# Kernel optimization log

Hardware: AMD Instinct MI355X
Metric: run time of the kernel (lower is better)

## Reference

```python
import jax, jax.numpy as jnp
import numpy as np
import math

CODE_NUM = 8192
GRAPH = 256
HID = 256
ATT = 128
TOUT = 256  # must equal HID (scattered into h_new)


def setup_inputs() -> dict:
    key = jax.random.key(0)
    ks = jax.random.split(key, 16)
    s = 0.02
    return {
        "m_embeddings": jax.random.normal(ks[0], (CODE_NUM, GRAPH), jnp.float32),
        "ddi_embeddings": jax.random.normal(ks[1], (CODE_NUM, GRAPH), jnp.float32),
        "unrelated_embeddings": jax.random.normal(ks[2], (CODE_NUM, GRAPH), jnp.float32),
        "hidden_state": jax.random.normal(ks[3], (CODE_NUM, HID), jnp.float32),
        # GRUCell params (torch layout: W_ih [3H, in], W_hh [3H, H])
        "W_ih": jax.random.normal(ks[4], (3 * HID, GRAPH), jnp.float32) * s,
        "W_hh": jax.random.normal(ks[5], (3 * HID, HID), jnp.float32) * s,
        "b_ih": jax.random.normal(ks[6], (3 * HID,), jnp.float32) * s,
        "b_hh": jax.random.normal(ks[7], (3 * HID,), jnp.float32) * s,
        # single-head attention params ([in, out] layout)
        "Wq": jax.random.normal(ks[8], (GRAPH, ATT), jnp.float32) * s,
        "bq": jax.random.normal(ks[9], (ATT,), jnp.float32) * s,
        "Wk": jax.random.normal(ks[10], (GRAPH, ATT), jnp.float32) * s,
        "bk": jax.random.normal(ks[11], (ATT,), jnp.float32) * s,
        "Wv": jax.random.normal(ks[12], (GRAPH, TOUT), jnp.float32) * s,
        "bv": jax.random.normal(ks[13], (TOUT,), jnp.float32) * s,
        # categorical group id per code: 0 -> m1 (GRU), 1 -> m2 (ddi), 2 -> m3 (unrelated)
        "divided": jax.random.randint(ks[14], (CODE_NUM,), 0, 3, jnp.int32),
    }


def reference(m_embeddings, ddi_embeddings, unrelated_embeddings, hidden_state,
              W_ih, W_hh, b_ih, b_hh, Wq, bq, Wk, bk, Wv, bv, divided):
    m1 = divided == 0
    m2 = divided == 1
    m3 = divided == 2
    m23 = m2 | m3

    # ---- GRUCell on all rows (row-independent); scatter only m1 rows ----
    gx = m_embeddings @ W_ih.T + b_ih          # [N, 3H]
    gh = hidden_state @ W_hh.T + b_hh          # [N, 3H]
    xr, xz, xn = jnp.split(gx, 3, axis=-1)
    hr, hz, hn = jnp.split(gh, 3, axis=-1)
    r = jax.nn.sigmoid(xr + hr)
    z = jax.nn.sigmoid(xz + hz)
    n = jnp.tanh(xn + r * hn)
    h_gru = (1.0 - z) * n + z * hidden_state   # [N, H]

    # ---- single-head attention over m2 u m3 subset (mask-based) ----
    q_in = jnp.where(m2[:, None], ddi_embeddings, unrelated_embeddings)  # [N, G]
    Q = q_in @ Wq + bq                          # [N, A]
    K = q_in @ Wk + bk                          # [N, A]
    V = m_embeddings @ Wv + bv                  # [N, TOUT]
    g = (Q @ K.T) / math.sqrt(ATT)              # [N, N]
    g = jnp.where(m23[None, :], g, -jnp.inf)    # keys restricted to m2 u m3
    score = jax.nn.softmax(g, axis=-1)
    h_m23 = jnp.tanh(score @ V)                 # [N, H]

    # ---- scatter into h_new ----
    h_new = jnp.where(m1[:, None], h_gru, 0.0)
    h_new = jnp.where(m23[:, None], h_m23, h_new)

    # ---- max-pooled outputs over each subset, then combined ----
    out1 = jnp.max(jnp.where(m1[:, None], h_gru, -jnp.inf), axis=0)    # [H]
    out23 = jnp.max(jnp.where(m23[:, None], h_m23, -jnp.inf), axis=0)  # [H]
    output = jnp.maximum(out1, out23)
    return output, h_new
```

## Files before the change

kernel.cpp:

```cpp
#include <hip/hip_runtime.h>

typedef __bf16 bf16_t;
typedef __bf16 bf16x8 __attribute__((ext_vector_type(8)));
typedef float f32x4 __attribute__((ext_vector_type(4)));

#define MFMA16(A, B, C) __builtin_amdgcn_mfma_f32_16x16x32_bf16(A, B, C, 0, 0, 0)

static constexpr int N_CODE = 8192;

static constexpr size_t OFF_B1   = 0;
static constexpr size_t OFF_B2   = OFF_B1 + 393216;
static constexpr size_t OFF_B3   = OFF_B2 + 393216;
static constexpr size_t OFF_BV   = OFF_B3 + 131072;
static constexpr size_t OFF_BIAS = OFF_BV + 131072;
static constexpr size_t OFF_U1   = OFF_BIAS + 8192;
static constexpr size_t OFF_U23  = OFF_U1 + 1024;
static constexpr size_t OFF_CNT  = OFF_U23 + 1024;
static constexpr size_t OFF_IDXS = OFF_CNT + 256;
static constexpr size_t OFF_IDXM = OFF_IDXS + 32768;
static constexpr size_t OFF_GXC  = OFF_IDXM + 32768;
static constexpr size_t OFF_GHC  = OFF_GXC + 12582912;
static constexpr size_t OFF_G3C  = OFF_GHC + 12582912;
static constexpr size_t OFF_VT   = OFF_G3C + 4194304;
static constexpr size_t OFF_KP   = OFF_VT + 4194304;
static constexpr size_t OFF_VP   = OFF_KP + 2097152;
static constexpr size_t OFF_PML  = OFF_VP + 4194304;
static constexpr size_t OFF_PO   = OFF_PML + 524288;

__device__ __forceinline__ unsigned umap_f(float f) {
    unsigned u = __float_as_uint(f);
    return (u & 0x80000000u) ? ~u : (u | 0x80000000u);
}
__device__ __forceinline__ float unmap_f(unsigned u) {
    unsigned b = (u & 0x80000000u) ? (u & 0x7fffffffu) : ~u;
    return __uint_as_float(b);
}

__global__ __launch_bounds__(1024)
void tl_prep_scan(const float* __restrict__ W_ih, const float* __restrict__ W_hh,
                  const float* __restrict__ Wq, const float* __restrict__ Wk,
                  const float* __restrict__ Wv,
                  const float* __restrict__ b_ih, const float* __restrict__ b_hh,
                  const float* __restrict__ bq, const float* __restrict__ bk,
                  const float* __restrict__ bv,
                  const int* __restrict__ divided,
                  bf16_t* __restrict__ B1p, bf16_t* __restrict__ B2p,
                  bf16_t* __restrict__ B3p, bf16_t* __restrict__ BVp,
                  float* __restrict__ biases,
                  unsigned* __restrict__ u1, unsigned* __restrict__ u23,
                  int* __restrict__ idxS, int* __restrict__ idxM1, int* __restrict__ counts)
{
    int t = threadIdx.x;
    if (blockIdx.x == 0) {
        __shared__ int w1[16], w23[16];
        int lane = t & 63, wv = t >> 6;
        int d[8]; int c1 = 0, c23 = 0;
#pragma unroll
        for (int i = 0; i < 8; ++i) {
            d[i] = divided[t*8 + i];
            c1  += (d[i] == 0);
            c23 += (d[i] != 0);
        }
        int s1v = c1, s23v = c23;
#pragma unroll
        for (int off = 1; off < 64; off <<= 1) {
            int a1  = __shfl_up(s1v,  off, 64);
            int a23 = __shfl_up(s23v, off, 64);
            if (lane >= off) { s1v += a1; s23v += a23; }
        }
        if (lane == 63) { w1[wv] = s1v; w23[wv] = s23v; }
        __syncthreads();
        if (wv == 0 && lane < 16) {
            int v1 = w1[lane], v23 = w23[lane];
#pragma unroll
            for (int off = 1; off < 16; off <<= 1) {
                int a1  = __shfl_up(v1,  off, 16);
                int a23 = __shfl_up(v23, off, 16);
                if (lane >= off) { v1 += a1; v23 += a23; }
            }
            w1[lane] = v1; w23[lane] = v23;
        }
        __syncthreads();
        int base1  = (wv > 0) ? w1[wv-1]  : 0;
        int base23 = (wv > 0) ? w23[wv-1] : 0;
        int o1  = base1  + s1v  - c1;
        int o23 = base23 + s23v - c23;
#pragma unroll
        for (int i = 0; i < 8; ++i) {
            if (d[i] == 0) idxM1[o1++] = t*8 + i;
            else           idxS[o23++] = t*8 + i;
        }
        if (t == 1023) { counts[0] = w23[15]; counts[1] = w1[15]; }
        return;
    }
    int idx = (blockIdx.x - 1) * 1024 + t;
    const int T1 = 196608, T2 = 196608, T3 = 65536, T4 = 65536;
    for (int i = idx; i < T1 + T2 + T3 + T4; i += 128 * 1024) {
        int which, l;
        if (i < T1)                { which = 0; l = i; }
        else if (i < T1 + T2)      { which = 1; l = i - T1; }
        else if (i < T1 + T2 + T3) { which = 2; l = i - T1 - T2; }
        else                       { which = 3; l = i - T1 - T2 - T3; }
        int j = l & 7, lane = (l >> 3) & 63, kk = (l >> 9) & 7, n16 = l >> 12;
        int k = kk*32 + (lane >> 4)*8 + j;
        int n = n16*16 + (lane & 15);
        if (which == 0)      B1p[l] = (bf16_t)W_ih[n*256 + k];
        else if (which == 1) B2p[l] = (bf16_t)W_hh[n*256 + k];
        else if (which == 2) B3p[l] = (bf16_t)((n < 128) ? Wq[k*128 + n] : Wk[k*128 + (n - 128)]);
        else                 BVp[l] = (bf16_t)Wv[k*256 + n];
    }
    if (idx < 768)       biases[idx] = b_ih[idx];
    else if (idx < 1536) biases[idx] = b_hh[idx - 768];
    else if (idx < 1792) { int q = idx - 1536; biases[idx] = (q < 128) ? bq[q] : bk[q - 128]; }
    else if (idx < 2048) biases[idx] = bv[idx - 1792];
    if (idx < 256) { u1[idx] = 0x007FFFFFu; u23[idx] = 0x007FFFFFu; }
}

__device__ __forceinline__ bf16x8 load_cvt8(const float* p) {
    f32x4 a = *(const f32x4*)p;
    f32x4 b = *(const f32x4*)(p + 4);
    bf16x8 r;
#pragma unroll
    for (int j = 0; j < 4; ++j) { r[j] = (bf16_t)a[j]; r[j+4] = (bf16_t)b[j]; }
    return r;
}

__global__ __launch_bounds__(256, 2)
void tl_gemm_quad(const float* __restrict__ m_emb, const float* __restrict__ hidden,
                  const float* __restrict__ ddi, const float* __restrict__ unrel,
                  const int* __restrict__ divided,
                  const bf16_t* __restrict__ B1p, const bf16_t* __restrict__ B2p,
                  const bf16_t* __restrict__ B3p, const bf16_t* __restrict__ BVp,
                  const float* __restrict__ biases,
                  bf16_t* __restrict__ gxc, bf16_t* __restrict__ ghc,
                  bf16_t* __restrict__ G3c, bf16_t* __restrict__ Vt,
                  const int* __restrict__ idxM1, const int* __restrict__ idxS,
                  const int* __restrict__ counts)
{
    int y = blockIdx.y;
    const float* A0; const float* A1 = nullptr; int mode = 0;
    const bf16_t* Bp; const float* bias; bf16_t* C; int NOUT; int y0;
    const int* gidx; int cnt;
    if (y < 3)       { A0 = m_emb;  gidx = idxM1; cnt = counts[1]; Bp = B1p; bias = biases;        C = gxc; NOUT = 768; y0 = y; }
    else if (y < 6)  { A0 = hidden; gidx = idxM1; cnt = counts[1]; Bp = B2p; bias = biases + 768;  C = ghc; NOUT = 768; y0 = y - 3; }
    else if (y == 6) { A0 = ddi; A1 = unrel; mode = 2;
                       gidx = idxS;  cnt = counts[0]; Bp = B3p; bias = biases + 1536; C = G3c; NOUT = 256; y0 = 0; }
    else             { A0 = m_emb;  gidx = idxS;  cnt = counts[0]; Bp = BVp; bias = biases + 1792; C = Vt;  NOUT = 256; y0 = 0; }

    int m0 = blockIdx.x * 64;
    if (m0 >= cnt) return;
    int lane = threadIdx.x & 63;
    int w    = threadIdx.x >> 6;
    int rlo = lane & 15, khi = lane >> 4;
    int nbase = y0 * 256 + w * 64;

    const float* arow[4];
#pragma unroll
    for (int m = 0; m < 4; ++m) {
        int row = m0 + m*16 + rlo;
        int src = gidx[(row < cnt) ? row : 0];
        const float* base = A0;
        if (mode == 2) base = (divided[src] == 1) ? A0 : A1;
        arow[m] = base + (size_t)src * 256;
    }
    f32x4 acc[4][4] = {};
    const bf16_t* bptr = Bp + (size_t)(nbase >> 4) * 4096 + lane * 8;
#pragma unroll
    for (int kk = 0; kk < 8; ++kk) {
        bf16x8 bfrag[4];
#pragma unroll
        for (int nf = 0; nf < 4; ++nf)
            bfrag[nf] = *(const bf16x8*)(bptr + nf * 4096 + kk * 512);
#pragma unroll
        for (int m = 0; m < 4; ++m) {
            bf16x8 afrag = load_cvt8(arow[m] + kk*32 + khi*8);
#pragma unroll
            for (int nf = 0; nf < 4; ++nf)
                acc[m][nf] = MFMA16(afrag, bfrag[nf], acc[m][nf]);
        }
    }
#pragma unroll
    for (int nf = 0; nf < 4; ++nf) {
        int col = nbase + nf*16 + rlo;
        float b = bias[col];
#pragma unroll
        for (int m = 0; m < 4; ++m)
#pragma unroll
            for (int r = 0; r < 4; ++r) {
                int row = m0 + m*16 + khi*4 + r;
                C[(size_t)row * NOUT + col] = (bf16_t)(acc[m][nf][r] + b);
            }
    }
}

__global__ __launch_bounds__(256)
void tl_gru_pack(const bf16_t* __restrict__ gx, const bf16_t* __restrict__ gh,
                 const float* __restrict__ hidden,
                 const int* __restrict__ idxM1, const int* __restrict__ counts,
                 float* __restrict__ h_new, unsigned* __restrict__ u1,
                 const bf16_t* __restrict__ G3c, const bf16_t* __restrict__ Vt,
                 bf16_t* __restrict__ Kp, bf16_t* __restrict__ Vp)
{
    if (blockIdx.x < 1024) {
        int nM1 = counts[1];
        int i0 = blockIdx.x * 8;
        if (i0 >= nM1) return;
        int j = threadIdx.x;
        int iend = (i0 + 8 < nM1) ? i0 + 8 : nM1;
        float cmax = -1e30f;
        for (int i = i0; i < iend; ++i) {
            int row = idxM1[i];
            float xr = (float)gx[(size_t)i*768 + j];
            float xz = (float)gx[(size_t)i*768 + 256 + j];
            float xn = (float)gx[(size_t)i*768 + 512 + j];
            float hr = (float)gh[(size_t)i*768 + j];
            float hz = (float)gh[(size_t)i*768 + 256 + j];
            float hn = (float)gh[(size_t)i*768 + 512 + j];
            float h  = hidden[(size_t)row*256 + j];
            float r = 1.f/(1.f + __expf(-(xr + hr)));
            float z = 1.f/(1.f + __expf(-(xz + hz)));
            float n = tanhf(xn + r*hn);
            float hg = (1.f - z)*n + z*h;
            h_new[(size_t)row*256 + j] = hg;
            cmax = fmaxf(cmax, hg);
        }
        atomicMax(&u1[j], umap_f(cmax));
        return;
    }
    int nS = counts[0];
    int nT = (nS + 63) >> 6;
    int r = (blockIdx.x - 1024) * 4 + (threadIdx.x >> 6);
    if (r >= nT * 64) return;
    int t = threadIdx.x & 63;
    bool valid = r < nS;
    if (t < 16) {
        bf16x8 v = {};
        if (valid) v = *(const bf16x8*)(G3c + (size_t)r*256 + 128 + t*8);
        int kt = r >> 6, keyin = r & 63;
        int ks = t >> 2, lhi = t & 3, nf = keyin >> 4;
        int lane = (lhi << 4) | (keyin & 15);
        *(bf16x8*)(Kp + ((((size_t)kt*4 + ks)*4 + nf)*64 + lane)*8) = v;
    } else if (t < 48) {
        int j8 = t - 16;
        int d0 = j8 * 8;
        bf16x8 v = {};
        if (valid) v = *(const bf16x8*)(Vt + (size_t)r*256 + d0);
        int kt = r >> 6, ks2 = (r >> 5) & 1, jj = r & 7, lhi = (r >> 3) & 3;
#pragma unroll
        for (int q = 0; q < 8; ++q) {
            int d = d0 + q;
            int nf = d >> 4;
            int lane = (lhi << 4) | (d & 15);
            Vp[((((size_t)kt*2 + ks2)*16 + nf)*64 + lane)*8 + jj] = v[q];
        }
    }
}

__global__ __launch_bounds__(256, 2)
void tl_attn(const bf16_t* __restrict__ G3c, const bf16_t* __restrict__ Kp,
             const bf16_t* __restrict__ Vp, const int* __restrict__ counts,
             int ksplit, float* __restrict__ pml, bf16_t* __restrict__ pO)
{
    int nS = counts[0];
    int nT = (nS + 63) >> 6;
    int qt = blockIdx.y;
    if (qt >= nT) return;
    int c = blockIdx.x;
    int kt0 = (nT * c) / ksplit, kt1 = (nT * (c + 1)) / ksplit;

    int lane = threadIdx.x & 63;
    int w    = threadIdx.x >> 6;
    int rlo = lane & 15, khi = lane >> 4;
    int qbase = qt * 64 + w * 16;

    __shared__ __align__(16) bf16_t P_lds[4][16][72];

    bf16x8 aQ[4];
    const bf16_t* qrow = G3c + (size_t)(qbase + rlo) * 256 + khi * 8;
#pragma unroll
    for (int ks = 0; ks < 4; ++ks) aQ[ks] = *(const bf16x8*)(qrow + ks * 32);

    float m_run[4], l_run[4];
#pragma unroll
    for (int r = 0; r < 4; ++r) { m_run[r] = -1e30f; l_run[r] = 0.f; }
    f32x4 O[16];
#pragma unroll
    for (int i = 0; i < 16; ++i) O[i] = (f32x4){0.f, 0.f, 0.f, 0.f};

    const float scale = 0.088388347648318447f;

    for (int kt = kt0; kt < kt1; ++kt) {
        f32x4 s[4] = {};
#pragma unroll
        for (int ks = 0; ks < 4; ++ks) {
            const bf16_t* kp = Kp + ((size_t)(kt*4 + ks) * 256 + lane) * 8;
#pragma unroll
            for (int nf = 0; nf < 4; ++nf) {
                bf16x8 bK = *(const bf16x8*)(kp + nf * 512);
                s[nf] = MFMA16(aQ[ks], bK, s[nf]);
            }
        }
        int kbase = kt * 64;
#pragma unroll
        for (int nf = 0; nf < 4; ++nf) {
            bool valid = (kbase + nf*16 + rlo) < nS;
#pragma unroll
            for (int r = 0; r < 4; ++r) {
                float v = s[nf][r] * scale;
                s[nf][r] = valid ? v : -1e30f;
            }
        }
        float pm[4];
#pragma unroll
        for (int r = 0; r < 4; ++r)
            pm[r] = fmaxf(fmaxf(s[0][r], s[1][r]), fmaxf(s[2][r], s[3][r]));
#pragma unroll
        for (int off = 1; off < 16; off <<= 1)
#pragma unroll
            for (int r = 0; r < 4; ++r) pm[r] = fmaxf(pm[r], __shfl_xor(pm[r], off, 64));

        float mn[4], sc[4], rs[4];
#pragma unroll
        for (int r = 0; r < 4; ++r) {
            mn[r] = fmaxf(m_run[r], pm[r]);
            sc[r] = __expf(m_run[r] - mn[r]);
            m_run[r] = mn[r];
            rs[r] = 0.f;
        }
#pragma unroll
        for (int nf = 0; nf < 4; ++nf)
#pragma unroll
            for (int r = 0; r < 4; ++r) {
                float p = __expf(s[nf][r] - mn[r]);
                s[nf][r] = p;
                rs[r] += p;
            }
#pragma unroll
        for (int off = 1; off < 16; off <<= 1)
#pragma unroll
            for (int r = 0; r < 4; ++r) rs[r] += __shfl_xor(rs[r], off, 64);
#pragma unroll
        for (int r = 0; r < 4; ++r) l_run[r] = l_run[r]*sc[r] + rs[r];
#pragma unroll
        for (int nf = 0; nf < 16; ++nf)
#pragma unroll
            for (int r = 0; r < 4; ++r) O[nf][r] *= sc[r];
#pragma unroll
        for (int nf = 0; nf < 4; ++nf)
#pragma unroll
            for (int r = 0; r < 4; ++r)
                P_lds[w][khi*4 + r][nf*16 + rlo] = (bf16_t)s[nf][r];
#pragma unroll
        for (int ks2 = 0; ks2 < 2; ++ks2) {
            bf16x8 pa = *(const bf16x8*)&P_lds[w][rlo][ks2*32 + khi*8];
            const bf16_t* vp = Vp + ((size_t)(kt*2 + ks2) * 1024 + lane) * 8;
#pragma unroll
            for (int nf = 0; nf < 16; ++nf) {
                bf16x8 bV = *(const bf16x8*)(vp + nf * 512);
                O[nf] = MFMA16(pa, bV, O[nf]);
            }
        }
    }
    if (rlo == 0) {
#pragma unroll
        for (int r = 0; r < 4; ++r) {
            int qc = qbase + khi*4 + r;
            pml[((size_t)c*N_CODE + qc)*2 + 0] = m_run[r];
            pml[((size_t)c*N_CODE + qc)*2 + 1] = l_run[r];
        }
    }
#pragma unroll
    for (int nf = 0; nf < 16; ++nf) {
        int d = nf*16 + rlo;
#pragma unroll
        for (int r = 0; r < 4; ++r) {
            int qc = qbase + khi*4 + r;
            pO[((size_t)c*N_CODE + qc)*256 + d] = (bf16_t)O[nf][r];
        }
    }
}

template<int KS>
__global__ __launch_bounds__(256)
void tl_merge_t(const bf16_t* __restrict__ pO, const float* __restrict__ pml,
                const int* __restrict__ idxS, const int* __restrict__ counts,
                float* __restrict__ h_new, unsigned* __restrict__ u23)
{
    int nS = counts[0];
    int i0 = blockIdx.x * 8;
    if (i0 >= nS) return;
    int tid = threadIdx.x;
    int qi = tid >> 5;
    int j8 = tid & 31;
    int q  = i0 + qi;

    __shared__ unsigned smax[256];
    smax[tid] = 0x007FFFFFu;
    __syncthreads();

    if (q < nS) {
        float m = -1e30f;
#pragma unroll
        for (int cc = 0; cc < KS; ++cc)
            m = fmaxf(m, pml[((size_t)cc*N_CODE + q)*2 + 0]);
        float e[KS]; float l = 0.f;
#pragma unroll
        for (int cc = 0; cc < KS; ++cc) {
            e[cc] = __expf(pml[((size_t)cc*N_CODE + q)*2 + 0] - m);
            l += pml[((size_t)cc*N_CODE + q)*2 + 1] * e[cc];
        }
        float acc[8] = {};
#pragma unroll
        for (int cc = 0; cc < KS; ++cc) {
            bf16x8 v = *(const bf16x8*)(pO + ((size_t)cc*N_CODE + q)*256 + j8*8);
#pragma unroll
            for (int k = 0; k < 8; ++k) acc[k] += (float)v[k] * e[cc];
        }
        float linv = 1.f / fmaxf(l, 1e-30f);
        f32x4 o0, o1;
#pragma unroll
        for (int k = 0; k < 8; ++k) {
            float val = tanhf(acc[k] * linv);
            if (k < 4) o0[k] = val; else o1[k-4] = val;
            atomicMax(&smax[j8*8 + k], umap_f(val));
        }
        float* dst = h_new + (size_t)idxS[q]*256 + j8*8;
        *(f32x4*)dst = o0;
        *(f32x4*)(dst + 4) = o1;
    }
    __syncthreads();
    atomicMax(&u23[tid], smax[tid]);
}

__global__ void tl_final(const unsigned* __restrict__ u1, const unsigned* __restrict__ u23,
                         float* __restrict__ out)
{
    int d = threadIdx.x;
    out[d] = fmaxf(unmap_f(u1[d]), unmap_f(u23[d]));
}

extern "C" void kernel_launch(void* const* d_in, const int* in_sizes, int n_in,
                              void* d_out, int out_size, void* d_ws, size_t ws_size,
                              hipStream_t stream) {
    const float* m_emb  = (const float*)d_in[0];
    const float* ddi    = (const float*)d_in[1];
    const float* unrel  = (const float*)d_in[2];
    const float* hidden = (const float*)d_in[3];
    const float* W_ih   = (const float*)d_in[4];
    const float* W_hh   = (const float*)d_in[5];
    const float* b_ih   = (const float*)d_in[6];
    const float* b_hh   = (const float*)d_in[7];
    const float* Wq     = (const float*)d_in[8];
    const float* bq     = (const float*)d_in[9];
    const float* Wk     = (const float*)d_in[10];
    const float* bk     = (const float*)d_in[11];
    const float* Wv     = (const float*)d_in[12];
    const float* bv     = (const float*)d_in[13];
    const int*   divided= (const int*)d_in[14];

    char* ws = (char*)d_ws;
    bf16_t* B1p   = (bf16_t*)(ws + OFF_B1);
    bf16_t* B2p   = (bf16_t*)(ws + OFF_B2);
    bf16_t* B3p   = (bf16_t*)(ws + OFF_B3);
    bf16_t* BVp   = (bf16_t*)(ws + OFF_BV);
    float*  biases= (float*)(ws + OFF_BIAS);
    unsigned* u1  = (unsigned*)(ws + OFF_U1);
    unsigned* u23 = (unsigned*)(ws + OFF_U23);
    int*    counts= (int*)(ws + OFF_CNT);
    int*    idxS  = (int*)(ws + OFF_IDXS);
    int*    idxM1 = (int*)(ws + OFF_IDXM);
    bf16_t* gxc   = (bf16_t*)(ws + OFF_GXC);
    bf16_t* ghc   = (bf16_t*)(ws + OFF_GHC);
    bf16_t* G3c   = (bf16_t*)(ws + OFF_G3C);
    bf16_t* Vt    = (bf16_t*)(ws + OFF_VT);
    bf16_t* Kp    = (bf16_t*)(ws + OFF_KP);
    bf16_t* Vp    = (bf16_t*)(ws + OFF_VP);
    float*  pml   = (float*)(ws + OFF_PML);
    bf16_t* pO    = (bf16_t*)(ws + OFF_PO);

    int ksplit;
    if (ws_size >= OFF_PO + (size_t)8 * 4194304)      ksplit = 8;
    else if (ws_size >= OFF_PO + (size_t)4 * 4194304) ksplit = 4;
    else                                              ksplit = 2;

    float* out   = (float*)d_out;
    float* h_new = out + 256;

    tl_prep_scan<<<dim3(129), dim3(1024), 0, stream>>>(W_ih, W_hh, Wq, Wk, Wv, b_ih, b_hh, bq, bk, bv,
                                                       divided, B1p, B2p, B3p, BVp, biases, u1, u23,
                                                       idxS, idxM1, counts);
    tl_gemm_quad<<<dim3(128, 8), dim3(256), 0, stream>>>(m_emb, hidden, ddi, unrel, divided,
                                                         B1p, B2p, B3p, BVp, biases,
                                                         gxc, ghc, G3c, Vt, idxM1, idxS, counts);
    tl_gru_pack<<<dim3(3072), dim3(256), 0, stream>>>(gxc, ghc, hidden, idxM1, counts, h_new, u1,
                                                      G3c, Vt, Kp, Vp);
    tl_attn<<<dim3(ksplit, 128), dim3(256), 0, stream>>>(G3c, Kp, Vp, counts, ksplit, pml, pO);
    if (ksplit == 8)      tl_merge_t<8><<<dim3(1024), dim3(256), 0, stream>>>(pO, pml, idxS, counts, h_new, u23);
    else if (ksplit == 4) tl_merge_t<4><<<dim3(1024), dim3(256), 0, stream>>>(pO, pml, idxS, counts, h_new, u23);
    else                  tl_merge_t<2><<<dim3(1024), dim3(256), 0, stream>>>(pO, pml, idxS, counts, h_new, u23);
    tl_final<<<dim3(1), dim3(256), 0, stream>>>(u1, u23, out);
}
```

Measured before the change: 147.1 us.

## Double-buffer K/V tiles in LDS via async global_load_lds in attention

```diff
diff --git a/kernel.cpp b/kernel.cpp
--- a/kernel.cpp
+++ b/kernel.cpp
@@ -3,6 +3,7 @@
 typedef __bf16 bf16_t;
 typedef __bf16 bf16x8 __attribute__((ext_vector_type(8)));
 typedef float f32x4 __attribute__((ext_vector_type(4)));
+typedef unsigned int u32;
 
 #define MFMA16(A, B, C) __builtin_amdgcn_mfma_f32_16x16x32_bf16(A, B, C, 0, 0, 0)
 
@@ -34,6 +35,13 @@
 __device__ __forceinline__ float unmap_f(unsigned u) {
     unsigned b = (u & 0x80000000u) ? (u & 0x7fffffffu) : ~u;
     return __uint_as_float(b);
+}
+
+__device__ __forceinline__ void gload16(const bf16_t* g, bf16_t* l) {
+    __builtin_amdgcn_global_load_lds(
+        (const __attribute__((address_space(1))) u32*)g,
+        (__attribute__((address_space(3))) u32*)l,
+        16, 0, 0);
 }
 
 __global__ __launch_bounds__(1024)
@@ -256,7 +264,7 @@
     }
 }
 
-__global__ __launch_bounds__(256, 2)
+__global__ __launch_bounds__(256)
 void tl_attn(const bf16_t* __restrict__ G3c, const bf16_t* __restrict__ Kp,
              const bf16_t* __restrict__ Vp, const int* __restrict__ counts,
              int ksplit, float* __restrict__ pml, bf16_t* __restrict__ pO)
@@ -268,11 +276,13 @@
     int c = blockIdx.x;
     int kt0 = (nT * c) / ksplit, kt1 = (nT * (c + 1)) / ksplit;
 
-    int lane = threadIdx.x & 63;
-    int w    = threadIdx.x >> 6;
+    int tid  = threadIdx.x;
+    int lane = tid & 63;
+    int w    = tid >> 6;
     int rlo = lane & 15, khi = lane >> 4;
     int qbase = qt * 64 + w * 16;
 
+    __shared__ __align__(16) bf16_t KV[2][24576];
     __shared__ __align__(16) bf16_t P_lds[4][16][72];
 
     bf16x8 aQ[4];
@@ -289,11 +299,32 @@
 
     const float scale = 0.088388347648318447f;
 
+    int cur = 0;
+    if (kt0 < kt1) {
+        const bf16_t* gK = Kp + (size_t)kt0 * 8192;
+        const bf16_t* gV = Vp + (size_t)kt0 * 16384;
+#pragma unroll
+        for (int i = 0; i < 4; ++i) gload16(gK + i*2048 + tid*8, &KV[0][i*2048 + w*512]);
+#pragma unroll
+        for (int i = 0; i < 8; ++i) gload16(gV + i*2048 + tid*8, &KV[0][8192 + i*2048 + w*512]);
+    }
+
     for (int kt = kt0; kt < kt1; ++kt) {
+        __syncthreads();
+        if (kt + 1 < kt1) {
+            const bf16_t* gK = Kp + (size_t)(kt+1) * 8192;
+            const bf16_t* gV = Vp + (size_t)(kt+1) * 16384;
+            bf16_t* nb = KV[cur ^ 1];
+#pragma unroll
+            for (int i = 0; i < 4; ++i) gload16(gK + i*2048 + tid*8, nb + i*2048 + w*512);
+#pragma unroll
+            for (int i = 0; i < 8; ++i) gload16(gV + i*2048 + tid*8, nb + 8192 + i*2048 + w*512);
+        }
+        const bf16_t* kvb = KV[cur];
         f32x4 s[4] = {};
 #pragma unroll
         for (int ks = 0; ks < 4; ++ks) {
-            const bf16_t* kp = Kp + ((size_t)(kt*4 + ks) * 256 + lane) * 8;
+            const bf16_t* kp = kvb + ks*2048 + lane*8;
 #pragma unroll
             for (int nf = 0; nf < 4; ++nf) {
                 bf16x8 bK = *(const bf16x8*)(kp + nf * 512);
@@ -353,13 +384,14 @@
 #pragma unroll
         for (int ks2 = 0; ks2 < 2; ++ks2) {
             bf16x8 pa = *(const bf16x8*)&P_lds[w][rlo][ks2*32 + khi*8];
-            const bf16_t* vp = Vp + ((size_t)(kt*2 + ks2) * 1024 + lane) * 8;
+            const bf16_t* vp = kvb + 8192 + ks2*8192 + lane*8;
 #pragma unroll
             for (int nf = 0; nf < 16; ++nf) {
                 bf16x8 bV = *(const bf16x8*)(vp + nf * 512);
                 O[nf] = MFMA16(pa, bV, O[nf]);
             }
         }
+        cur ^= 1;
     }
     if (rlo == 0) {
 #pragma unroll
```

New measurement: 166.6 us. 1.13x slower.
